# Kernel tuning notes

Hardware: AMD Instinct MI355X
Metric: run time of the kernel (lower is better)

The kernel has to match this reference:

```python
import jax, jax.numpy as jnp
import numpy as np

B, S, H, E = 4, 4096, 4096, 64
EPS = 1e-6


def setup_inputs() -> dict:
    key = jax.random.key(0)
    k1, k2 = jax.random.split(key)
    hidden_states = jax.random.normal(k1, (B, S, H), dtype=jnp.float32)
    gate_w = jax.random.normal(k2, (E, H), dtype=jnp.float32) * 0.02
    return {"hidden_states": hidden_states, "gate_w": gate_w, "C": 512}


def reference(hidden_states, gate_w, C):
    b, s, h = hidden_states.shape
    e = gate_w.shape[0]
    flat = hidden_states.reshape(-1, h)                    # [BS, H]
    logits = jnp.einsum('th,eh->te', flat, gate_w)          # [BS, E]
    # deterministic=True -> no noise added
    probs = jax.nn.softmax(logits, axis=-1)                 # [BS, E]
    # expert-choice: each expert picks top-C tokens
    _, topC_idx = jax.lax.top_k(logits.T, C)                # [E, C] token indices
    routing_map = jnp.zeros_like(logits).at[
        topC_idx, jnp.arange(e)[:, None]].set(1.0)          # [BS, E]
    # normalize_weights=True
    probs = probs * routing_map
    probs = probs / (probs.sum(axis=-1, keepdims=True) + EPS)
    # aux losses (torch .std() is unbiased -> ddof=1)
    importance = probs.sum(axis=0)                          # [E]
    imp_loss = (jnp.std(importance, ddof=1) / (importance.mean() + EPS)) ** 2
    load = routing_map.sum(axis=0)                          # [E]
    load_loss = (jnp.std(load, ddof=1) / (load.mean() + EPS)) ** 2
    aux_loss = imp_loss + load_loss
    return (probs.reshape(b, s, e), routing_map.reshape(b, s, e), aux_loss)
```

## Files before the change

### kernel.cpp

```cpp
#include <hip/hip_runtime.h>
#include <hip/hip_bf16.h>

#define BS 16384
#define HDIM 4096
#define NE 64
#define KC 64
#define TT 32
#define CAP 512
#define DELTA 2e-3f

typedef __bf16 bf16x8 __attribute__((ext_vector_type(8)));
typedef float f32x4 __attribute__((ext_vector_type(4)));
union Frag { uint4 q; bf16x8 v; };

__device__ inline unsigned f2key(float f) {
    unsigned u = __float_as_uint(f);
    return (u & 0x80000000u) ? ~u : (u | 0x80000000u);
}
__device__ inline float key2f(unsigned k) {
    unsigned u = (k & 0x80000000u) ? (k ^ 0x80000000u) : ~k;
    return __uint_as_float(u);
}
__device__ inline unsigned pack_hi(float a, float b) {
    return (__float_as_uint(a) >> 16) | (__float_as_uint(b) & 0xFFFF0000u);
}
__device__ inline float bf16_resid(float a) {
    return a - __uint_as_float(__float_as_uint(a) & 0xFFFF0000u);
}

__global__ __launch_bounds__(256) void k0_init(const float* __restrict__ W,
                                               unsigned short* __restrict__ Wh,
                                               unsigned short* __restrict__ Wl,
                                               unsigned long long* __restrict__ win_t) {
    const int gtid = blockIdx.x * 256 + threadIdx.x;
    const size_t f = (size_t)gtid * 4;
    float4 w = *(const float4*)(W + f);
    uint2 hh, ll;
    hh.x = pack_hi(w.x, w.y); hh.y = pack_hi(w.z, w.w);
    ll.x = pack_hi(bf16_resid(w.x), bf16_resid(w.y));
    ll.y = pack_hi(bf16_resid(w.z), bf16_resid(w.w));
    *(uint2*)(Wh + f) = hh;
    *(uint2*)(Wl + f) = ll;
    if (gtid < BS) win_t[gtid] = 0ull;
}

__global__ __launch_bounds__(256, 2) void k1_gemm(const float* __restrict__ A,
                                                  const unsigned short* __restrict__ Wh,
                                                  const unsigned short* __restrict__ Wl,
                                                  float* __restrict__ Lg,
                                                  unsigned* __restrict__ KeyT) {
    __shared__ __align__(16) unsigned short sbuf[2 * 13824];

    const int tid = threadIdx.x;
    const int T0 = blockIdx.x * TT;

    const int arow = tid >> 3, aseg = tid & 7;

    const int lane = tid & 63, w = tid >> 6;
    const int m = lane & 15, q = lane >> 4;
    const int wm = w & 1;
    const int wn = w >> 1;

    const float* Aprow = A + (size_t)(T0 + arow) * HDIM + aseg * 8;

    f32x4 acc[2] = {{0.f, 0.f, 0.f, 0.f}, {0.f, 0.f, 0.f, 0.f}};

    float4 pa0 = *(const float4*)(Aprow);
    float4 pa1 = *(const float4*)(Aprow + 4);
    uint4 pwh[2], pwl[2];
#pragma unroll
    for (int i = 0; i < 2; ++i) {
        const int u = i * 256 + tid;
        const int r = u >> 3, blk = u & 7;
        pwh[i] = *(const uint4*)(Wh + (size_t)r * HDIM + blk * 8);
        pwl[i] = *(const uint4*)(Wl + (size_t)r * HDIM + blk * 8);
    }

    {
        unsigned short* B = sbuf;
        uint4 H, L;
        H.x = pack_hi(pa0.x, pa0.y); H.y = pack_hi(pa0.z, pa0.w);
        H.z = pack_hi(pa1.x, pa1.y); H.w = pack_hi(pa1.z, pa1.w);
        L.x = pack_hi(bf16_resid(pa0.x), bf16_resid(pa0.y));
        L.y = pack_hi(bf16_resid(pa0.z), bf16_resid(pa0.w));
        L.z = pack_hi(bf16_resid(pa1.x), bf16_resid(pa1.y));
        L.w = pack_hi(bf16_resid(pa1.z), bf16_resid(pa1.w));
        *(uint4*)(B + arow * 72 + aseg * 8) = H;
        *(uint4*)(B + 2304 + arow * 72 + aseg * 8) = L;
#pragma unroll
        for (int i = 0; i < 2; ++i) {
            const int u = i * 256 + tid;
            const int r = u >> 3, blk = u & 7;
            *(uint4*)(B + 4608 + r * 72 + blk * 8) = pwh[i];
            *(uint4*)(B + 9216 + r * 72 + blk * 8) = pwl[i];
        }
    }

    for (int c = 0; c < HDIM / KC; ++c) {
        if (c + 1 < HDIM / KC) {
            const int c0 = (c + 1) * KC;
            pa0 = *(const float4*)(Aprow + c0);
            pa1 = *(const float4*)(Aprow + c0 + 4);
#pragma unroll
            for (int i = 0; i < 2; ++i) {
                const int u = i * 256 + tid;
                const int r = u >> 3, blk = u & 7;
                pwh[i] = *(const uint4*)(Wh + (size_t)r * HDIM + c0 + blk * 8);
                pwl[i] = *(const uint4*)(Wl + (size_t)r * HDIM + c0 + blk * 8);
            }
        }
        __syncthreads();
        {
            const unsigned short* B = sbuf + (c & 1) * 13824;
            const unsigned short* Ash = B + (wm * 16 + m) * 72;
            const unsigned short* Asl = Ash + 2304;
#pragma unroll
            for (int kh = 0; kh < 2; ++kh) {
                const int ko = kh * 32 + q * 8;
                Frag ah, al;
                ah.q = *(const uint4*)(Ash + ko);
                al.q = *(const uint4*)(Asl + ko);
#pragma unroll
                for (int nt = 0; nt < 2; ++nt) {
                    const int er = wn * 32 + nt * 16 + m;
                    Frag bh, bl;
                    bh.q = *(const uint4*)(B + 4608 + er * 72 + ko);
                    bl.q = *(const uint4*)(B + 9216 + er * 72 + ko);
                    acc[nt] = __builtin_amdgcn_mfma_f32_16x16x32_bf16(ah.v, bh.v, acc[nt], 0, 0, 0);
                    acc[nt] = __builtin_amdgcn_mfma_f32_16x16x32_bf16(al.v, bh.v, acc[nt], 0, 0, 0);
                    acc[nt] = __builtin_amdgcn_mfma_f32_16x16x32_bf16(ah.v, bl.v, acc[nt], 0, 0, 0);
                }
            }
        }
        if (c + 1 < HDIM / KC) {
            unsigned short* B = sbuf + ((c + 1) & 1) * 13824;
            uint4 H, L;
            H.x = pack_hi(pa0.x, pa0.y); H.y = pack_hi(pa0.z, pa0.w);
            H.z = pack_hi(pa1.x, pa1.y); H.w = pack_hi(pa1.z, pa1.w);
            L.x = pack_hi(bf16_resid(pa0.x), bf16_resid(pa0.y));
            L.y = pack_hi(bf16_resid(pa0.z), bf16_resid(pa0.w));
            L.z = pack_hi(bf16_resid(pa1.x), bf16_resid(pa1.y));
            L.w = pack_hi(bf16_resid(pa1.z), bf16_resid(pa1.w));
            *(uint4*)(B + arow * 72 + aseg * 8) = H;
            *(uint4*)(B + 2304 + arow * 72 + aseg * 8) = L;
#pragma unroll
            for (int i = 0; i < 2; ++i) {
                const int u = i * 256 + tid;
                const int r = u >> 3, blk = u & 7;
                *(uint4*)(B + 4608 + r * 72 + blk * 8) = pwh[i];
                *(uint4*)(B + 9216 + r * 72 + blk * 8) = pwl[i];
            }
        }
    }

    __syncthreads();
    float* Sc = (float*)sbuf;
#pragma unroll
    for (int nt = 0; nt < 2; ++nt) {
        const int e = wn * 32 + nt * 16 + m;
#pragma unroll
        for (int r = 0; r < 4; ++r) {
            const int tl = wm * 16 + q * 4 + r;
            const float v = acc[nt][r];
            Sc[tl * 68 + e] = v;
            Lg[(size_t)(T0 + tl) * NE + e] = v;
        }
    }
    __syncthreads();
    {
        const int e = tid >> 2, jj = tid & 3;
        unsigned kk[8];
#pragma unroll
        for (int r = 0; r < 8; ++r) kk[r] = f2key(Sc[(jj * 8 + r) * 68 + e]);
        uint4 v0 = {kk[0], kk[1], kk[2], kk[3]}, v1 = {kk[4], kk[5], kk[6], kk[7]};
        unsigned* dst = KeyT + (size_t)e * BS + T0 + jj * 8;
        *(uint4*)dst = v0;
        *(uint4*)(dst + 4) = v1;
    }
}

__global__ __launch_bounds__(1024) void k2_select(const unsigned* __restrict__ KeyT,
                                                  const int* __restrict__ Cptr,
                                                  unsigned* __restrict__ khi_g,
                                                  int* __restrict__ needed_g,
                                                  int* __restrict__ ncand_g,
                                                  int* __restrict__ cand_g) {
    const int e = blockIdx.x, tid = threadIdx.x;
    const int wid = tid >> 6, lane = tid & 63;
    const int C = *Cptr;
    const unsigned* col = KeyT + (size_t)e * BS;

    unsigned key[16];
#pragma unroll
    for (int j = 0; j < 16; ++j) key[j] = col[j * 1024 + tid];

    __shared__ int sred[16];
    __shared__ int s_tot;
    __shared__ int s_nc;

    unsigned K = 0;
    for (int b = 31; b >= 0; --b) {
        const unsigned T = K | (1u << b);
        int c = 0;
#pragma unroll
        for (int j = 0; j < 16; ++j) c += (key[j] >= T);
#pragma unroll
        for (int off = 32; off; off >>= 1) c += __shfl_xor(c, off);
        if (lane == 0) sred[wid] = c;
        __syncthreads();
        if (wid == 0) {
            int v = (lane < 16) ? sred[lane] : 0;
            v += __shfl_xor(v, 1); v += __shfl_xor(v, 2);
            v += __shfl_xor(v, 4); v += __shfl_xor(v, 8);
            if (lane == 0) s_tot = v;
        }
        __syncthreads();
        if (s_tot >= C) K = T;
        __syncthreads();
    }

    const float vT = key2f(K);
    const unsigned khi = f2key(vT + DELTA);
    const unsigned klo = f2key(vT - DELTA);

    int nd = 0;
#pragma unroll
    for (int j = 0; j < 16; ++j) nd += (key[j] > khi);
#pragma unroll
    for (int off = 32; off; off >>= 1) nd += __shfl_xor(nd, off);
    if (lane == 0) sred[wid] = nd;
    if (tid == 0) s_nc = 0;
    __syncthreads();
    if (wid == 0) {
        int v = (lane < 16) ? sred[lane] : 0;
        v += __shfl_xor(v, 1); v += __shfl_xor(v, 2);
        v += __shfl_xor(v, 4); v += __shfl_xor(v, 8);
        if (lane == 0) s_tot = v;
    }
    __syncthreads();
#pragma unroll
    for (int j = 0; j < 16; ++j) {
        if (key[j] >= klo && key[j] <= khi) {
            const int pos = atomicAdd(&s_nc, 1);
            if (pos < CAP) cand_g[(size_t)e * CAP + pos] = j * 1024 + tid;
        }
    }
    __syncthreads();
    if (tid == 0) {
        khi_g[e] = khi;
        needed_g[e] = C - s_tot;
        ncand_g[e] = (s_nc < CAP) ? s_nc : CAP;
    }
}

__global__ __launch_bounds__(256) void k2b_resolve(const float* __restrict__ A,
                                                   const float* __restrict__ W,
                                                   const int* __restrict__ needed_g,
                                                   const int* __restrict__ ncand_g,
                                                   const int* __restrict__ cand_g,
                                                   unsigned long long* __restrict__ win_t) {
    const int e = blockIdx.x, tid = threadIdx.x, w = tid >> 6, lane = tid & 63;
    int n = ncand_g[e]; if (n > CAP) n = CAP;
    int need = needed_g[e]; if (need > n) need = n; if (need < 0) need = 0;
    __shared__ double sval[CAP];
    __shared__ int sidx[CAP];
    const float* Wr = W + (size_t)e * HDIM;
    for (int c = w; c < n; c += 4) {
        const int t = cand_g[(size_t)e * CAP + c];
        const float* Ar = A + (size_t)t * HDIM;
        double ps = 0.0;
#pragma unroll 8
        for (int j = 0; j < HDIM / 64; ++j)
            ps += (double)Ar[j * 64 + lane] * (double)Wr[j * 64 + lane];
#pragma unroll
        for (int off = 32; off; off >>= 1) ps += __shfl_xor(ps, off);
        if (lane == 0) { sval[c] = ps; sidx[c] = t; }
    }
    __syncthreads();
    if (tid == 0) {
        for (int s = 0; s < need; ++s) {
            int best = -1;
            for (int c = 0; c < n; ++c) {
                if (sidx[c] < 0) continue;
                if (best < 0 || sval[c] > sval[best] ||
                    (sval[c] == sval[best] && sidx[c] < sidx[best]))
                    best = c;
            }
            const int t = sidx[best];
            atomicOr(&win_t[t], 1ull << e);
            sidx[best] = -1;
        }
    }
}

__global__ __launch_bounds__(256) void k3_softmax(const float* __restrict__ Lg,
                                                  const unsigned* __restrict__ khi_g,
                                                  const unsigned long long* __restrict__ win_t,
                                                  float* __restrict__ probs,
                                                  float* __restrict__ out_map,
                                                  double* __restrict__ imp_partial) {
    const int tid = threadIdx.x, w = tid >> 6, e = tid & 63, b = blockIdx.x;
    __shared__ unsigned skhi[64];
    __shared__ double sim[4][64];
    if (tid < 64) skhi[tid] = khi_g[tid];
    __syncthreads();
    const unsigned kh = skhi[e];
    double accim = 0.0;
#pragma unroll
    for (int it = 0; it < 16; ++it) {
        const int t = b * 64 + it * 4 + w;
        const float x = Lg[(size_t)t * NE + e];
        const unsigned key = f2key(x);
        float mfl;
        if (key > kh) mfl = 1.f;
        else mfl = (float)((win_t[t] >> e) & 1ull);
        const float ev = expf(x);
        const float evm = ev * mfl;
        float s1 = ev, s2 = evm;
#pragma unroll
        for (int off = 32; off; off >>= 1) {
            s1 += __shfl_xor(s1, off);
            s2 += __shfl_xor(s2, off);
        }
        const float o = evm / (s2 + 1e-6f * s1);
        probs[(size_t)t * NE + e] = o;
        out_map[(size_t)t * NE + e] = mfl;
        accim += (double)o;
    }
    sim[w][e] = accim;
    __syncthreads();
    if (w == 0)
        imp_partial[(size_t)b * NE + e] = sim[0][e] + sim[1][e] + sim[2][e] + sim[3][e];
}

__global__ __launch_bounds__(64) void k4_aux(const double* __restrict__ imp_partial,
                                             float* __restrict__ out_aux) {
    const int e = threadIdx.x;
    double v = 0.0;
    for (int b = 0; b < 256; ++b) v += imp_partial[(size_t)b * NE + e];
    double s = v;
#pragma unroll
    for (int off = 32; off; off >>= 1) s += __shfl_xor(s, off);
    const double mean = s / 64.0;
    const double d = v - mean;
    double ss = d * d;
#pragma unroll
    for (int off = 32; off; off >>= 1) ss += __shfl_xor(ss, off);
    if (e == 0) {
        const double var = ss / 63.0;
        const double dn = mean + 1e-6;
        out_aux[0] = (float)(var / (dn * dn));
    }
}

extern "C" void kernel_launch(void* const* d_in, const int* in_sizes, int n_in,
                              void* d_out, int out_size, void* d_ws, size_t ws_size,
                              hipStream_t stream) {
    const float* A = (const float*)d_in[0];
    const float* W = (const float*)d_in[1];
    const int* Cptr = (const int*)d_in[2];

    float* out_probs = (float*)d_out;
    float* out_map = out_probs + (size_t)BS * NE;
    float* out_aux = out_map + (size_t)BS * NE;

    char* wsb = (char*)d_ws;
    float*              Lg     = (float*)wsb;
    unsigned*           KeyT   = (unsigned*)(wsb + (4ull << 20));
    unsigned short*     Wh     = (unsigned short*)(wsb + (8ull << 20));
    unsigned short*     Wl     = (unsigned short*)(wsb + (8ull << 20) + (512ull << 10));
    int*                cand   = (int*)(wsb + (9ull << 20));
    unsigned long long* win_t  = (unsigned long long*)(wsb + (9ull << 20) + (128ull << 10));
    unsigned*           khi_g  = (unsigned*)(wsb + (9ull << 20) + (256ull << 10));
    int*                needed = (int*)(wsb + (9ull << 20) + (257ull << 10));
    int*                ncand  = (int*)(wsb + (9ull << 20) + (258ull << 10));
    double*             imp_p  = (double*)(wsb + (9ull << 20) + (512ull << 10));

    k0_init<<<256, 256, 0, stream>>>(W, Wh, Wl, win_t);
    k1_gemm<<<BS / TT, 256, 0, stream>>>(A, Wh, Wl, Lg, KeyT);
    k2_select<<<NE, 1024, 0, stream>>>(KeyT, Cptr, khi_g, needed, ncand, cand);
    k2b_resolve<<<NE, 256, 0, stream>>>(A, W, needed, ncand, cand, win_t);
    k3_softmax<<<BS / 64, 256, 0, stream>>>(Lg, khi_g, win_t, out_probs, out_map, imp_p);
    k4_aux<<<1, 64, 0, stream>>>(imp_p, out_aux);
}
```

Measured before the change: 455.6 us.

## Fuse select with resolve, fold aux into softmax, shorten radix threshold search

Merges the per-expert threshold selection and the fp64 candidate re-scoring into one kernel, with candidates kept in shared memory. The radix search now runs 16 levels instead of 32, tries a shortcut that starts at bit 22 when the threshold lies in a known exponent range, and counts with shared-memory atomics. The softmax kernel uses 4x more blocks, and the last block to finish (tracked by a global counter) computes the aux loss, so the separate aux kernel is gone. Together these cut two launches and several barriers. The cost is a wider candidate window and a last-block reduction that is serial over 1024 partials.

Result: slower. 563.7 us (+23.7%).

```diff
diff --git a/kernel.cpp b/kernel.cpp
--- a/kernel.cpp
+++ b/kernel.cpp
@@ -8,6 +8,7 @@
 #define TT 32
 #define CAP 512
 #define DELTA 2e-3f
+#define K3B 1024
 
 typedef __bf16 bf16x8 __attribute__((ext_vector_type(8)));
 typedef float f32x4 __attribute__((ext_vector_type(4)));
@@ -31,7 +32,8 @@
 __global__ __launch_bounds__(256) void k0_init(const float* __restrict__ W,
                                                unsigned short* __restrict__ Wh,
                                                unsigned short* __restrict__ Wl,
-                                               unsigned long long* __restrict__ win_t) {
+                                               unsigned long long* __restrict__ win_t,
+                                               unsigned* __restrict__ counter) {
     const int gtid = blockIdx.x * 256 + threadIdx.x;
     const size_t f = (size_t)gtid * 4;
     float4 w = *(const float4*)(W + f);
@@ -42,6 +44,7 @@
     *(uint2*)(Wh + f) = hh;
     *(uint2*)(Wl + f) = ll;
     if (gtid < BS) win_t[gtid] = 0ull;
+    if (gtid == 0) *counter = 0u;
 }
 
 __global__ __launch_bounds__(256, 2) void k1_gemm(const float* __restrict__ A,
@@ -179,12 +182,12 @@
     }
 }
 
-__global__ __launch_bounds__(1024) void k2_select(const unsigned* __restrict__ KeyT,
-                                                  const int* __restrict__ Cptr,
-                                                  unsigned* __restrict__ khi_g,
-                                                  int* __restrict__ needed_g,
-                                                  int* __restrict__ ncand_g,
-                                                  int* __restrict__ cand_g) {
+__global__ __launch_bounds__(1024) void k2_fused(const unsigned* __restrict__ KeyT,
+                                                 const int* __restrict__ Cptr,
+                                                 const float* __restrict__ A,
+                                                 const float* __restrict__ W,
+                                                 unsigned* __restrict__ khi_g,
+                                                 unsigned long long* __restrict__ win_t) {
     const int e = blockIdx.x, tid = threadIdx.x;
     const int wid = tid >> 6, lane = tid & 63;
     const int C = *Cptr;
@@ -192,81 +195,62 @@
 
     unsigned key[16];
 #pragma unroll
-    for (int j = 0; j < 16; ++j) key[j] = col[j * 1024 + tid];
-
-    __shared__ int sred[16];
-    __shared__ int s_tot;
+    for (int j4 = 0; j4 < 4; ++j4) {
+        const uint4 v = *(const uint4*)(col + j4 * 4096 + tid * 4);
+        key[j4 * 4 + 0] = v.x; key[j4 * 4 + 1] = v.y;
+        key[j4 * 4 + 2] = v.z; key[j4 * 4 + 3] = v.w;
+    }
+
+    __shared__ int s_arr[20];
     __shared__ int s_nc;
-
-    unsigned K = 0;
-    for (int b = 31; b >= 0; --b) {
+    __shared__ int sidx[CAP];
+    __shared__ double sval[CAP];
+    if (tid < 20) s_arr[tid] = 0;
+    if (tid == 0) s_nc = 0;
+    __syncthreads();
+
+    int step = 0;
+    auto bcount = [&](unsigned T) -> int {
+        int c = 0;
+#pragma unroll
+        for (int j = 0; j < 16; ++j) c += (key[j] >= T);
+#pragma unroll
+        for (int off = 32; off; off >>= 1) c += __shfl_xor(c, off);
+        if (lane == 0) atomicAdd(&s_arr[step], c);
+        __syncthreads();
+        return s_arr[step++];
+    };
+
+    const int cLo = bcount(0xC0000000u);
+    const int cHi = bcount(0xC0800000u);
+    unsigned K; int bstart;
+    if (cLo >= C && cHi < C) { K = 0xC0000000u; bstart = 22; }
+    else                     { K = 0u;          bstart = 31; }
+    for (int b = bstart; b >= 15; --b) {
         const unsigned T = K | (1u << b);
-        int c = 0;
-#pragma unroll
-        for (int j = 0; j < 16; ++j) c += (key[j] >= T);
-#pragma unroll
-        for (int off = 32; off; off >>= 1) c += __shfl_xor(c, off);
-        if (lane == 0) sred[wid] = c;
-        __syncthreads();
-        if (wid == 0) {
-            int v = (lane < 16) ? sred[lane] : 0;
-            v += __shfl_xor(v, 1); v += __shfl_xor(v, 2);
-            v += __shfl_xor(v, 4); v += __shfl_xor(v, 8);
-            if (lane == 0) s_tot = v;
-        }
-        __syncthreads();
-        if (s_tot >= C) K = T;
-        __syncthreads();
-    }
-
-    const float vT = key2f(K);
-    const unsigned khi = f2key(vT + DELTA);
-    const unsigned klo = f2key(vT - DELTA);
-
-    int nd = 0;
-#pragma unroll
-    for (int j = 0; j < 16; ++j) nd += (key[j] > khi);
-#pragma unroll
-    for (int off = 32; off; off >>= 1) nd += __shfl_xor(nd, off);
-    if (lane == 0) sred[wid] = nd;
-    if (tid == 0) s_nc = 0;
-    __syncthreads();
-    if (wid == 0) {
-        int v = (lane < 16) ? sred[lane] : 0;
-        v += __shfl_xor(v, 1); v += __shfl_xor(v, 2);
-        v += __shfl_xor(v, 4); v += __shfl_xor(v, 8);
-        if (lane == 0) s_tot = v;
-    }
-    __syncthreads();
+        if (bcount(T) >= C) K = T;
+    }
+    const float vlo = key2f(K);
+    const float vhi = key2f(K + 0x8000u);
+    const unsigned khi = f2key(vhi + DELTA);
+    const unsigned klo = f2key(vlo - DELTA);
+    const int nd = bcount(khi + 1u);
+    int need = C - nd;
+
 #pragma unroll
     for (int j = 0; j < 16; ++j) {
         if (key[j] >= klo && key[j] <= khi) {
             const int pos = atomicAdd(&s_nc, 1);
-            if (pos < CAP) cand_g[(size_t)e * CAP + pos] = j * 1024 + tid;
-        }
-    }
-    __syncthreads();
-    if (tid == 0) {
-        khi_g[e] = khi;
-        needed_g[e] = C - s_tot;
-        ncand_g[e] = (s_nc < CAP) ? s_nc : CAP;
-    }
-}
-
-__global__ __launch_bounds__(256) void k2b_resolve(const float* __restrict__ A,
-                                                   const float* __restrict__ W,
-                                                   const int* __restrict__ needed_g,
-                                                   const int* __restrict__ ncand_g,
-                                                   const int* __restrict__ cand_g,
-                                                   unsigned long long* __restrict__ win_t) {
-    const int e = blockIdx.x, tid = threadIdx.x, w = tid >> 6, lane = tid & 63;
-    int n = ncand_g[e]; if (n > CAP) n = CAP;
-    int need = needed_g[e]; if (need > n) need = n; if (need < 0) need = 0;
-    __shared__ double sval[CAP];
-    __shared__ int sidx[CAP];
+            if (pos < CAP) sidx[pos] = (j >> 2) * 4096 + tid * 4 + (j & 3);
+        }
+    }
+    __syncthreads();
+    int n = s_nc; if (n > CAP) n = CAP;
+    if (need > n) need = n; if (need < 0) need = 0;
+
     const float* Wr = W + (size_t)e * HDIM;
-    for (int c = w; c < n; c += 4) {
-        const int t = cand_g[(size_t)e * CAP + c];
+    for (int c = wid; c < n; c += 16) {
+        const int t = sidx[c];
         const float* Ar = A + (size_t)t * HDIM;
         double ps = 0.0;
 #pragma unroll 8
@@ -274,10 +258,11 @@
             ps += (double)Ar[j * 64 + lane] * (double)Wr[j * 64 + lane];
 #pragma unroll
         for (int off = 32; off; off >>= 1) ps += __shfl_xor(ps, off);
-        if (lane == 0) { sval[c] = ps; sidx[c] = t; }
+        if (lane == 0) sval[c] = ps;
     }
     __syncthreads();
     if (tid == 0) {
+        khi_g[e] = khi;
         for (int s = 0; s < need; ++s) {
             int best = -1;
             for (int c = 0; c < n; ++c) {
@@ -286,8 +271,7 @@
                     (sval[c] == sval[best] && sidx[c] < sidx[best]))
                     best = c;
             }
-            const int t = sidx[best];
-            atomicOr(&win_t[t], 1ull << e);
+            atomicOr(&win_t[sidx[best]], 1ull << e);
             sidx[best] = -1;
         }
     }
@@ -298,17 +282,20 @@
                                                   const unsigned long long* __restrict__ win_t,
                                                   float* __restrict__ probs,
                                                   float* __restrict__ out_map,
-                                                  double* __restrict__ imp_partial) {
+                                                  double* __restrict__ imp_partial,
+                                                  unsigned* __restrict__ counter,
+                                                  float* __restrict__ out_aux) {
     const int tid = threadIdx.x, w = tid >> 6, e = tid & 63, b = blockIdx.x;
     __shared__ unsigned skhi[64];
     __shared__ double sim[4][64];
+    __shared__ int s_last;
     if (tid < 64) skhi[tid] = khi_g[tid];
     __syncthreads();
     const unsigned kh = skhi[e];
     double accim = 0.0;
 #pragma unroll
-    for (int it = 0; it < 16; ++it) {
-        const int t = b * 64 + it * 4 + w;
+    for (int it = 0; it < 4; ++it) {
+        const int t = b * 16 + it * 4 + w;
         const float x = Lg[(size_t)t * NE + e];
         const unsigned key = f2key(x);
         float mfl;
@@ -331,25 +318,33 @@
     __syncthreads();
     if (w == 0)
         imp_partial[(size_t)b * NE + e] = sim[0][e] + sim[1][e] + sim[2][e] + sim[3][e];
-}
-
-__global__ __launch_bounds__(64) void k4_aux(const double* __restrict__ imp_partial,
-                                             float* __restrict__ out_aux) {
-    const int e = threadIdx.x;
+    __threadfence();
+    __syncthreads();
+    if (tid == 0) s_last = (atomicAdd(counter, 1u) == gridDim.x - 1);
+    __syncthreads();
+    if (!s_last) return;
+    __threadfence();
+
     double v = 0.0;
-    for (int b = 0; b < 256; ++b) v += imp_partial[(size_t)b * NE + e];
-    double s = v;
-#pragma unroll
-    for (int off = 32; off; off >>= 1) s += __shfl_xor(s, off);
-    const double mean = s / 64.0;
-    const double d = v - mean;
-    double ss = d * d;
-#pragma unroll
-    for (int off = 32; off; off >>= 1) ss += __shfl_xor(ss, off);
-    if (e == 0) {
-        const double var = ss / 63.0;
-        const double dn = mean + 1e-6;
-        out_aux[0] = (float)(var / (dn * dn));
+    for (int bb = w; bb < (int)gridDim.x; bb += 4)
+        v += imp_partial[(size_t)bb * NE + e];
+    sim[w][e] = v;
+    __syncthreads();
+    if (w == 0) {
+        const double ve = sim[0][e] + sim[1][e] + sim[2][e] + sim[3][e];
+        double s = ve;
+#pragma unroll
+        for (int off = 32; off; off >>= 1) s += __shfl_xor(s, off);
+        const double mean = s / 64.0;
+        const double d = ve - mean;
+        double ss = d * d;
+#pragma unroll
+        for (int off = 32; off; off >>= 1) ss += __shfl_xor(ss, off);
+        if (e == 0) {
+            const double var = ss / 63.0;
+            const double dn = mean + 1e-6;
+            out_aux[0] = (float)(var / (dn * dn));
+        }
     }
 }
 
@@ -369,17 +364,14 @@
     unsigned*           KeyT   = (unsigned*)(wsb + (4ull << 20));
     unsigned short*     Wh     = (unsigned short*)(wsb + (8ull << 20));
     unsigned short*     Wl     = (unsigned short*)(wsb + (8ull << 20) + (512ull << 10));
-    int*                cand   = (int*)(wsb + (9ull << 20));
-    unsigned long long* win_t  = (unsigned long long*)(wsb + (9ull << 20) + (128ull << 10));
-    unsigned*           khi_g  = (unsigned*)(wsb + (9ull << 20) + (256ull << 10));
-    int*                needed = (int*)(wsb + (9ull << 20) + (257ull << 10));
-    int*                ncand  = (int*)(wsb + (9ull << 20) + (258ull << 10));
-    double*             imp_p  = (double*)(wsb + (9ull << 20) + (512ull << 10));
-
-    k0_init<<<256, 256, 0, stream>>>(W, Wh, Wl, win_t);
+    unsigned long long* win_t  = (unsigned long long*)(wsb + (9ull << 20));
+    unsigned*           khi_g  = (unsigned*)(wsb + (9ull << 20) + (128ull << 10));
+    unsigned*           counter= (unsigned*)(wsb + (9ull << 20) + (132ull << 10));
+    double*             imp_p  = (double*)(wsb + (9ull << 20) + (256ull << 10));
+
+    k0_init<<<256, 256, 0, stream>>>(W, Wh, Wl, win_t, counter);
     k1_gemm<<<BS / TT, 256, 0, stream>>>(A, Wh, Wl, Lg, KeyT);
-    k2_select<<<NE, 1024, 0, stream>>>(KeyT, Cptr, khi_g, needed, ncand, cand);
-    k2b_resolve<<<NE, 256, 0, stream>>>(A, W, needed, ncand, cand, win_t);
-    k3_softmax<<<BS / 64, 256, 0, stream>>>(Lg, khi_g, win_t, out_probs, out_map, imp_p);
-    k4_aux<<<1, 64, 0, stream>>>(imp_p, out_aux);
-}
+    k2_fused<<<NE, 1024, 0, stream>>>(KeyT, Cptr, A, W, khi_g, win_t);
+    k3_softmax<<<K3B, 256, 0, stream>>>(Lg, khi_g, win_t, out_probs, out_map, imp_p,
+                                        counter, out_aux);
+}
```
